# Kernel optimization log

Hardware: AMD Instinct MI355X
Metric: run time of the kernel (lower is better)

The kernel has to match this reference:

```python
import jax, jax.numpy as jnp
import numpy as np


def _lstm_cell(gates, c_prev):
    # PyTorch gate order: input, forget, cell(g), output
    i, f, g, o = jnp.split(gates, 4, axis=-1)
    c = jax.nn.sigmoid(f) * c_prev + jax.nn.sigmoid(i) * jnp.tanh(g)
    h = jax.nn.sigmoid(o) * jnp.tanh(c)
    return h, c


def setup_inputs() -> dict:
    key = jax.random.key(0)
    ks = jax.random.split(key, 20)
    s = 0.1
    x = jax.random.normal(ks[0], (1, 1, 37), dtype=jnp.float32)
    # active flags live at columns 12 + 5*opp_id; set opponents 0,2,3 active (==1)
    act_idx = 12 + 5 * jnp.arange(5)
    flags = jnp.array([1.0, 0.0, 1.0, 1.0, 0.0], dtype=jnp.float32)
    x = x.at[0, 0, act_idx].set(flags)
    inp = {
        'x': x,
        'gen_Wih': s * jax.random.normal(ks[1], (10, 40, 12), dtype=jnp.float32),
        'gen_Whh': s * jax.random.normal(ks[2], (10, 40, 10), dtype=jnp.float32),
        'gen_bih': s * jax.random.normal(ks[3], (10, 40), dtype=jnp.float32),
        'gen_bhh': s * jax.random.normal(ks[4], (10, 40), dtype=jnp.float32),
        'gen_h0': s * jax.random.normal(ks[5], (10, 10), dtype=jnp.float32),
        'gen_c0': s * jax.random.normal(ks[6], (10, 10), dtype=jnp.float32),
        'game_Wih': s * jax.random.normal(ks[7], (5, 10, 20, 4), dtype=jnp.float32),
        'game_Whh': s * jax.random.normal(ks[8], (5, 10, 20, 5), dtype=jnp.float32),
        'game_bih': s * jax.random.normal(ks[9], (5, 10, 20), dtype=jnp.float32),
        'game_bhh': s * jax.random.normal(ks[10], (5, 10, 20), dtype=jnp.float32),
        'game_h0': s * jax.random.normal(ks[11], (5, 10, 5), dtype=jnp.float32),
        'game_c0': s * jax.random.normal(ks[12], (5, 10, 5), dtype=jnp.float32),
        'W1': s * jax.random.normal(ks[13], (50, 200), dtype=jnp.float32),
        'b1': s * jax.random.normal(ks[14], (50,), dtype=jnp.float32),
        'W2': s * jax.random.normal(ks[15], (10, 50), dtype=jnp.float32),
        'b2': s * jax.random.normal(ks[16], (10,), dtype=jnp.float32),
        'W3': s * jax.random.normal(ks[17], (1, 10), dtype=jnp.float32),
        'b3': s * jax.random.normal(ks[18], (1,), dtype=jnp.float32),
    }
    return inp


def reference(x, gen_Wih, gen_Whh, gen_bih, gen_bhh, gen_h0, gen_c0,
              game_Wih, game_Whh, game_bih, game_bhh, game_h0, game_c0,
              W1, b1, W2, b2, W3, b3):
    # seq_len = batch = 1 (forced by the view(1,1,-1) -> Linear(200) shapes)
    xg = x[0, 0, :12]                                     # [12] general features
    # 10 independent LSTM(12,10) cells, batched via einsum over the cell axis k
    gates_g = (jnp.einsum('kgd,d->kg', gen_Wih, xg)
               + jnp.einsum('kgh,kh->kg', gen_Whh, gen_h0)
               + gen_bih + gen_bhh)                       # [10, 40]
    h_gen, _ = _lstm_cell(gates_g, gen_c0)                # [10, 10]
    x_gen_out = h_gen.reshape(-1)                         # [100]

    xo = x[0, 0, 12:37].reshape(5, 5)                     # 5 opponents x 5 feats
    active = xo[:, 0]                                     # active flag
    feats = xo[:, 1:]                                     # [5, 4]
    # 5 opponents x 10 independent LSTM(4,5) game cells
    gates_o = (jnp.einsum('okgd,od->okg', game_Wih, feats)
               + jnp.einsum('okgh,okh->okg', game_Whh, game_h0)
               + game_bih + game_bhh)                     # [5, 10, 20]
    h_game, _ = _lstm_cell(gates_o, game_c0)              # [5, 10, 5]
    game_flat = h_game.reshape(5, 50)
    # Bug replicated from source: the round loop concatenates x_opp_game (the
    # stale output of game-LSTM #9) 10 times; round LSTM outputs are unused.
    repeated = jnp.tile(h_game[:, 9, :], (1, 10))         # [5, 50]
    opp_single = jnp.concatenate([game_flat, repeated], axis=1)  # [5, 100]

    mask = (active == 1.0).astype(x.dtype)                # 'if x_active == 1'
    opp_avg = (mask[:, None] * opp_single).sum(0) / mask.sum()   # mean over active

    test = jnp.concatenate([x_gen_out, opp_avg])          # [200]
    h1 = jnp.tanh(test @ W1.T + b1)
    h2 = jnp.tanh(h1 @ W2.T + b2)
    out = jnp.tanh(h2 @ W3.T + b3)
    return out.reshape(1, 1, 1)
```

## Files before the change

### kernel.cpp

```cpp
#include <hip/hip_runtime.h>
#include <math.h>


__device__ __forceinline__ float fsig(float v) {
    return __fdividef(1.0f, 1.0f + __expf(-v));
}
__device__ __forceinline__ float ftanh(float v) {
    return 1.0f - __fdividef(2.0f, 1.0f + __expf(2.0f * v));
}

__global__ __launch_bounds__(1024) void net6max_kernel(
    const float* __restrict__ x,
    const float* __restrict__ gen_Wih,
    const float* __restrict__ gen_Whh,
    const float* __restrict__ gen_bih,
    const float* __restrict__ gen_bhh,
    const float* __restrict__ gen_h0,
    const float* __restrict__ gen_c0,
    const float* __restrict__ game_Wih,
    const float* __restrict__ game_Whh,
    const float* __restrict__ game_bih,
    const float* __restrict__ game_bhh,
    const float* __restrict__ game_h0,
    const float* __restrict__ game_c0,
    const float* __restrict__ W1,
    const float* __restrict__ b1,
    const float* __restrict__ W2,
    const float* __restrict__ b2,
    const float* __restrict__ W3,
    const float* __restrict__ b3,
    float* __restrict__ out)
{
    __shared__ __align__(16) float s_xg[12];
    __shared__ __align__(16) float s_feats[5][4];
    __shared__ __align__(16) float s_active[8];
    __shared__ __align__(16) float s_gates_g[400];
    __shared__ __align__(16) float s_gates_o[1000];
    __shared__ __align__(16) float s_hgame[5][10][5];
    __shared__ __align__(16) float s_test[200];
    __shared__ __align__(16) float s_h1[52];
    __shared__ __align__(16) float s_h2[12];

    const int tid = threadIdx.x;

    if (tid < 12) s_xg[tid] = x[tid];
    if (tid >= 64 && tid < 64 + 25) {
        int j = tid - 64;
        int o = j / 5, c = j % 5;
        float v = x[12 + j];
        if (c == 0) s_active[o] = v;
        else        s_feats[o][c - 1] = v;
    }
    __syncthreads();

    if (tid < 400) {
        int k = tid / 40;
        const float4* wih4 = (const float4*)(gen_Wih + (size_t)tid * 12);
        const float2* whh2 = (const float2*)(gen_Whh + (size_t)tid * 10);
        const float2* h02  = (const float2*)(gen_h0 + k * 10);
        float4 xa = *(const float4*)&s_xg[0];
        float4 xb = *(const float4*)&s_xg[4];
        float4 xc = *(const float4*)&s_xg[8];
        float4 p4 = wih4[0] * xa + wih4[1] * xb + wih4[2] * xc;
        float2 q2 = whh2[0] * h02[0] + whh2[1] * h02[1] + whh2[2] * h02[2]
                  + whh2[3] * h02[3] + whh2[4] * h02[4];
        float acc = gen_bih[tid] + gen_bhh[tid]
                  + p4.x + p4.y + p4.z + p4.w + q2.x + q2.y;
        s_gates_g[tid] = acc;
    }

    {
        int gt = -1;
        if (tid < 400)       gt = 600 + tid;
        else if (tid >= 424) gt = tid - 424;
        if (gt >= 0) {
            int o   = gt / 200;
            int ok_ = gt / 20;
            const float4* wih4 = (const float4*)(game_Wih + (size_t)gt * 4);
            const float*  whh  = game_Whh + (size_t)gt * 5;
            const float*  h0   = game_h0 + ok_ * 5;
            float4 f4 = *(const float4*)&s_feats[o][0];
            float4 p  = wih4[0] * f4;
            float acc = game_bih[gt] + game_bhh[gt] + p.x + p.y + p.z + p.w;
            acc += whh[0]*h0[0] + whh[1]*h0[1] + whh[2]*h0[2]
                 + whh[3]*h0[3] + whh[4]*h0[4];
            s_gates_o[gt] = acc;
        }
    }
    __syncthreads();

    if (tid < 100) {
        int k = tid / 10, j = tid % 10;
        int base = k * 40;
        float gi = s_gates_g[base + j];
        float gf = s_gates_g[base + 10 + j];
        float gg = s_gates_g[base + 20 + j];
        float go = s_gates_g[base + 30 + j];
        float c = fsig(gf) * gen_c0[tid] + fsig(gi) * ftanh(gg);
        s_test[tid] = fsig(go) * ftanh(c);
    } else if (tid >= 512 && tid < 512 + 250) {
        int t = tid - 512;
        int o = t / 50;
        int rem = t % 50;
        int k = rem / 5, j = rem % 5;
        int base = (o * 10 + k) * 20;
        float gi = s_gates_o[base + j];
        float gf = s_gates_o[base + 5 + j];
        float gg = s_gates_o[base + 10 + j];
        float go = s_gates_o[base + 15 + j];
        float c = fsig(gf) * game_c0[(o * 10 + k) * 5 + j] + fsig(gi) * ftanh(gg);
        s_hgame[o][k][j] = fsig(go) * ftanh(c);
    }
    __syncthreads();

    if (tid < 100) {
        float msum = 0.0f, acc = 0.0f;
        #pragma unroll
        for (int o = 0; o < 5; ++o) {
            float m = (s_active[o] == 1.0f) ? 1.0f : 0.0f;
            msum += m;
            float v = (tid < 50) ? s_hgame[o][tid / 5][tid % 5]
                                 : s_hgame[o][9][(tid - 50) % 5];
            acc += m * v;
        }
        s_test[100 + tid] = __fdividef(acc, msum);
    }
    __syncthreads();

    if (tid < 200) {
        int r = tid >> 2, q = tid & 3;
        const float4* w4 = (const float4*)(W1 + (size_t)r * 200);
        const float4* t4 = (const float4*)s_test;
        float4 acc4 = make_float4(0.f, 0.f, 0.f, 0.f);
        #pragma unroll
        for (int m = 0; m < 12; ++m) {
            int c4 = q + 4 * m;
            acc4 += w4[c4] * t4[c4];
        }
        if (q < 2) {
            int c4 = 48 + q;
            acc4 += w4[c4] * t4[c4];
        }
        float acc = acc4.x + acc4.y + acc4.z + acc4.w;
        acc += __shfl_xor(acc, 1);
        acc += __shfl_xor(acc, 2);
        if (q == 0) s_h1[r] = ftanh(acc + b1[r]);
    }
    __syncthreads();

    if (tid < 20) {
        int r = tid >> 1, q = tid & 1;
        const float2* w2 = (const float2*)(W2 + (size_t)r * 50);
        const float2* h2 = (const float2*)s_h1;
        float2 acc2 = make_float2(0.f, 0.f);
        #pragma unroll
        for (int m = 0; m < 12; ++m) {
            int c = q + 2 * m;
            acc2 += w2[c] * h2[c];
        }
        if (q == 0) acc2 += w2[24] * h2[24];
        float acc = acc2.x + acc2.y;
        acc += __shfl_xor(acc, 1);
        if (q == 0) s_h2[r] = ftanh(acc + b2[r]);
    }
    __syncthreads();

    if (tid == 0) {
        float acc = b3[0];
        #pragma unroll
        for (int c = 0; c < 10; ++c) acc += W3[c] * s_h2[c];
        out[0] = ftanh(acc);
    }
}

extern "C" void kernel_launch(void* const* d_in, const int* in_sizes, int n_in,
                              void* d_out, int out_size, void* d_ws, size_t ws_size,
                              hipStream_t stream) {
    (void)in_sizes; (void)n_in; (void)out_size; (void)d_ws; (void)ws_size;
    const float* x        = (const float*)d_in[0];
    const float* gen_Wih  = (const float*)d_in[1];
    const float* gen_Whh  = (const float*)d_in[2];
    const float* gen_bih  = (const float*)d_in[3];
    const float* gen_bhh  = (const float*)d_in[4];
    const float* gen_h0   = (const float*)d_in[5];
    const float* gen_c0   = (const float*)d_in[6];
    const float* game_Wih = (const float*)d_in[7];
    const float* game_Whh = (const float*)d_in[8];
    const float* game_bih = (const float*)d_in[9];
    const float* game_bhh = (const float*)d_in[10];
    const float* game_h0  = (const float*)d_in[11];
    const float* game_c0  = (const float*)d_in[12];
    const float* W1       = (const float*)d_in[13];
    const float* b1       = (const float*)d_in[14];
    const float* W2       = (const float*)d_in[15];
    const float* b2       = (const float*)d_in[16];
    const float* W3       = (const float*)d_in[17];
    const float* b3       = (const float*)d_in[18];
    float* out = (float*)d_out;

    net6max_kernel<<<1, 1024, 0, stream>>>(
        x, gen_Wih, gen_Whh, gen_bih, gen_bhh, gen_h0, gen_c0,
        game_Wih, game_Whh, game_bih, game_bhh, game_h0, game_c0,
        W1, b1, W2, b2, W3, b3, out);
}
```

Baseline: 10.71 us.

## Fuse LSTM gate matvecs into cell threads and shrink block to 384

Each LSTM cell thread now computes its own four gate dot products directly from global memory instead of staging gates in shared memory, which removes two barriers and the input staging step. The block shrinks from 1024 to 384 threads. The final W2 and W3 layers are merged through a warp shuffle reduction, removing one more barrier and the s_h2 buffer. Each thread now does four times the gate work serially, so the critical path gets longer per thread in exchange for fewer syncs.

```diff
diff --git a/kernel.cpp b/kernel.cpp
--- a/kernel.cpp
+++ b/kernel.cpp
@@ -9,7 +9,7 @@
     return 1.0f - __fdividef(2.0f, 1.0f + __expf(2.0f * v));
 }
 
-__global__ __launch_bounds__(1024) void net6max_kernel(
+__global__ __launch_bounds__(384) void net6max_kernel(
     const float* __restrict__ x,
     const float* __restrict__ gen_Wih,
     const float* __restrict__ gen_Whh,
@@ -31,85 +31,63 @@
     const float* __restrict__ b3,
     float* __restrict__ out)
 {
-    __shared__ __align__(16) float s_xg[12];
-    __shared__ __align__(16) float s_feats[5][4];
-    __shared__ __align__(16) float s_active[8];
-    __shared__ __align__(16) float s_gates_g[400];
-    __shared__ __align__(16) float s_gates_o[1000];
     __shared__ __align__(16) float s_hgame[5][10][5];
     __shared__ __align__(16) float s_test[200];
     __shared__ __align__(16) float s_h1[52];
-    __shared__ __align__(16) float s_h2[12];
 
     const int tid = threadIdx.x;
 
-    if (tid < 12) s_xg[tid] = x[tid];
-    if (tid >= 64 && tid < 64 + 25) {
-        int j = tid - 64;
-        int o = j / 5, c = j % 5;
-        float v = x[12 + j];
-        if (c == 0) s_active[o] = v;
-        else        s_feats[o][c - 1] = v;
-    }
-    __syncthreads();
-
-    if (tid < 400) {
-        int k = tid / 40;
-        const float4* wih4 = (const float4*)(gen_Wih + (size_t)tid * 12);
-        const float2* whh2 = (const float2*)(gen_Whh + (size_t)tid * 10);
-        const float2* h02  = (const float2*)(gen_h0 + k * 10);
-        float4 xa = *(const float4*)&s_xg[0];
-        float4 xb = *(const float4*)&s_xg[4];
-        float4 xc = *(const float4*)&s_xg[8];
-        float4 p4 = wih4[0] * xa + wih4[1] * xb + wih4[2] * xc;
-        float2 q2 = whh2[0] * h02[0] + whh2[1] * h02[1] + whh2[2] * h02[2]
-                  + whh2[3] * h02[3] + whh2[4] * h02[4];
-        float acc = gen_bih[tid] + gen_bhh[tid]
-                  + p4.x + p4.y + p4.z + p4.w + q2.x + q2.y;
-        s_gates_g[tid] = acc;
-    }
-
-    {
-        int gt = -1;
-        if (tid < 400)       gt = 600 + tid;
-        else if (tid >= 424) gt = tid - 424;
-        if (gt >= 0) {
-            int o   = gt / 200;
-            int ok_ = gt / 20;
-            const float4* wih4 = (const float4*)(game_Wih + (size_t)gt * 4);
-            const float*  whh  = game_Whh + (size_t)gt * 5;
-            const float*  h0   = game_h0 + ok_ * 5;
-            float4 f4 = *(const float4*)&s_feats[o][0];
-            float4 p  = wih4[0] * f4;
-            float acc = game_bih[gt] + game_bhh[gt] + p.x + p.y + p.z + p.w;
-            acc += whh[0]*h0[0] + whh[1]*h0[1] + whh[2]*h0[2]
-                 + whh[3]*h0[3] + whh[4]*h0[4];
-            s_gates_o[gt] = acc;
-        }
-    }
-    __syncthreads();
-
     if (tid < 100) {
         int k = tid / 10, j = tid % 10;
-        int base = k * 40;
-        float gi = s_gates_g[base + j];
-        float gf = s_gates_g[base + 10 + j];
-        float gg = s_gates_g[base + 20 + j];
-        float go = s_gates_g[base + 30 + j];
-        float c = fsig(gf) * gen_c0[tid] + fsig(gi) * ftanh(gg);
-        s_test[tid] = fsig(go) * ftanh(c);
-    } else if (tid >= 512 && tid < 512 + 250) {
-        int t = tid - 512;
-        int o = t / 50;
-        int rem = t % 50;
+        const float*  Wk  = gen_Wih + (size_t)k * 480;
+        const float*  Uk  = gen_Whh + (size_t)k * 400;
+        const float*  bi  = gen_bih + k * 40;
+        const float*  bh  = gen_bhh + k * 40;
+        const float2* h02 = (const float2*)(gen_h0 + k * 10);
+        float2 h0a = h02[0], h0b = h02[1], h0c = h02[2], h0d = h02[3], h0e = h02[4];
+        float4 xa = *(const float4*)&x[0];
+        float4 xb = *(const float4*)&x[4];
+        float4 xc = *(const float4*)&x[8];
+        float g4[4];
+        #pragma unroll
+        for (int gq = 0; gq < 4; ++gq) {
+            int r = gq * 10 + j;
+            const float4* w4 = (const float4*)(Wk + r * 12);
+            const float2* u2 = (const float2*)(Uk + r * 10);
+            float4 p = w4[0] * xa + w4[1] * xb + w4[2] * xc;
+            float2 q = u2[0] * h0a + u2[1] * h0b + u2[2] * h0c
+                     + u2[3] * h0d + u2[4] * h0e;
+            g4[gq] = bi[r] + bh[r] + p.x + p.y + p.z + p.w + q.x + q.y;
+        }
+        float c = fsig(g4[1]) * gen_c0[tid] + fsig(g4[0]) * ftanh(g4[2]);
+        s_test[tid] = fsig(g4[3]) * ftanh(c);
+    } else if (tid >= 128 && tid < 378) {
+        int u = tid - 128;
+        int o = u / 50;
+        int rem = u % 50;
         int k = rem / 5, j = rem % 5;
-        int base = (o * 10 + k) * 20;
-        float gi = s_gates_o[base + j];
-        float gf = s_gates_o[base + 5 + j];
-        float gg = s_gates_o[base + 10 + j];
-        float go = s_gates_o[base + 15 + j];
-        float c = fsig(gf) * game_c0[(o * 10 + k) * 5 + j] + fsig(gi) * ftanh(gg);
-        s_hgame[o][k][j] = fsig(go) * ftanh(c);
+        int ok = o * 10 + k;
+        const float* Wk = game_Wih + (size_t)ok * 80;
+        const float* Uk = game_Whh + (size_t)ok * 100;
+        const float* bi = game_bih + ok * 20;
+        const float* bh = game_bhh + ok * 20;
+        const float* h0 = game_h0 + ok * 5;
+        float h00 = h0[0], h01 = h0[1], h02_ = h0[2], h03 = h0[3], h04 = h0[4];
+        const float* fx = x + 13 + 5 * o;
+        float f0 = fx[0], f1 = fx[1], f2 = fx[2], f3 = fx[3];
+        float g4[4];
+        #pragma unroll
+        for (int gq = 0; gq < 4; ++gq) {
+            int r = gq * 5 + j;
+            float4 w = *(const float4*)(Wk + r * 4);
+            const float* uu = Uk + r * 5;
+            float acc = bi[r] + bh[r]
+                      + w.x * f0 + w.y * f1 + w.z * f2 + w.w * f3;
+            acc += uu[0]*h00 + uu[1]*h01 + uu[2]*h02_ + uu[3]*h03 + uu[4]*h04;
+            g4[gq] = acc;
+        }
+        float c = fsig(g4[1]) * game_c0[ok * 5 + j] + fsig(g4[0]) * ftanh(g4[2]);
+        s_hgame[o][k][j] = fsig(g4[3]) * ftanh(c);
     }
     __syncthreads();
 
@@ -117,10 +95,10 @@
         float msum = 0.0f, acc = 0.0f;
         #pragma unroll
         for (int o = 0; o < 5; ++o) {
-            float m = (s_active[o] == 1.0f) ? 1.0f : 0.0f;
+            float m = (x[12 + 5 * o] == 1.0f) ? 1.0f : 0.0f;
             msum += m;
             float v = (tid < 50) ? s_hgame[o][tid / 5][tid % 5]
-                                 : s_hgame[o][9][(tid - 50) % 5];
+                                 : s_hgame[o][9][tid % 5];
             acc += m * v;
         }
         s_test[100 + tid] = __fdividef(acc, msum);
@@ -148,28 +126,29 @@
     }
     __syncthreads();
 
-    if (tid < 20) {
-        int r = tid >> 1, q = tid & 1;
-        const float2* w2 = (const float2*)(W2 + (size_t)r * 50);
-        const float2* h2 = (const float2*)s_h1;
-        float2 acc2 = make_float2(0.f, 0.f);
-        #pragma unroll
-        for (int m = 0; m < 12; ++m) {
-            int c = q + 2 * m;
-            acc2 += w2[c] * h2[c];
+    if (tid < 32) {
+        float acc = 0.f;
+        if (tid < 20) {
+            int r = tid >> 1, q = tid & 1;
+            const float2* w2 = (const float2*)(W2 + (size_t)r * 50);
+            const float2* h1v = (const float2*)s_h1;
+            float2 acc2 = make_float2(0.f, 0.f);
+            #pragma unroll
+            for (int m = 0; m < 12; ++m) {
+                int c = q + 2 * m;
+                acc2 += w2[c] * h1v[c];
+            }
+            if (q == 0) acc2 += w2[24] * h1v[24];
+            float a = acc2.x + acc2.y;
+            a += __shfl_xor(a, 1);
+            acc = (q == 0) ? ftanh(a + b2[r]) * W3[r] : 0.f;
         }
-        if (q == 0) acc2 += w2[24] * h2[24];
-        float acc = acc2.x + acc2.y;
+        acc += __shfl_xor(acc, 2);
+        acc += __shfl_xor(acc, 4);
+        acc += __shfl_xor(acc, 8);
+        acc += __shfl_xor(acc, 16);
         acc += __shfl_xor(acc, 1);
-        if (q == 0) s_h2[r] = ftanh(acc + b2[r]);
-    }
-    __syncthreads();
-
-    if (tid == 0) {
-        float acc = b3[0];
-        #pragma unroll
-        for (int c = 0; c < 10; ++c) acc += W3[c] * s_h2[c];
-        out[0] = ftanh(acc);
+        if (tid == 0) out[0] = ftanh(acc + b3[0]);
     }
 }
 
@@ -198,7 +177,7 @@
     const float* b3       = (const float*)d_in[18];
     float* out = (float*)d_out;
 
-    net6max_kernel<<<1, 1024, 0, stream>>>(
+    net6max_kernel<<<1, 384, 0, stream>>>(
         x, gen_Wih, gen_Whh, gen_bih, gen_bhh, gen_h0, gen_c0,
         game_Wih, game_Whh, game_bih, game_bhh, game_h0, game_c0,
         W1, b1, W2, b2, W3, b3, out);
```

Result: faster. 9.558 us (-10.7%).

## Prefetch MLP weights into LDS early and drop staging syncs

Applied to the files above, without the earlier changes.

Loads W1 and W2 into shared memory during the gate-computation phase, so their global-memory latency overlaps with the LSTM work instead of sitting on the later serial MLP path. Removes the initial shared staging of x and its barrier by reading x straight from global memory. Fuses the final W3 dot product into the W2 stage with a warp shuffle reduction, removing one barrier and a serial loop. The cost is a larger LDS footprint and more global loads issued at the start, plus a padded W1 row stride to avoid bank conflicts.

```diff
diff --git a/kernel.cpp b/kernel.cpp
--- a/kernel.cpp
+++ b/kernel.cpp
@@ -31,44 +31,30 @@
     const float* __restrict__ b3,
     float* __restrict__ out)
 {
-    __shared__ __align__(16) float s_xg[12];
-    __shared__ __align__(16) float s_feats[5][4];
-    __shared__ __align__(16) float s_active[8];
+    __shared__ __align__(16) float4 s_W1v[50 * 51];
+    __shared__ __align__(16) float2 s_W2v[10 * 25];
     __shared__ __align__(16) float s_gates_g[400];
     __shared__ __align__(16) float s_gates_o[1000];
     __shared__ __align__(16) float s_hgame[5][10][5];
     __shared__ __align__(16) float s_test[200];
     __shared__ __align__(16) float s_h1[52];
-    __shared__ __align__(16) float s_h2[12];
 
     const int tid = threadIdx.x;
-
-    if (tid < 12) s_xg[tid] = x[tid];
-    if (tid >= 64 && tid < 64 + 25) {
-        int j = tid - 64;
-        int o = j / 5, c = j % 5;
-        float v = x[12 + j];
-        if (c == 0) s_active[o] = v;
-        else        s_feats[o][c - 1] = v;
-    }
-    __syncthreads();
 
     if (tid < 400) {
         int k = tid / 40;
         const float4* wih4 = (const float4*)(gen_Wih + (size_t)tid * 12);
         const float2* whh2 = (const float2*)(gen_Whh + (size_t)tid * 10);
         const float2* h02  = (const float2*)(gen_h0 + k * 10);
-        float4 xa = *(const float4*)&s_xg[0];
-        float4 xb = *(const float4*)&s_xg[4];
-        float4 xc = *(const float4*)&s_xg[8];
+        float4 xa = *(const float4*)&x[0];
+        float4 xb = *(const float4*)&x[4];
+        float4 xc = *(const float4*)&x[8];
         float4 p4 = wih4[0] * xa + wih4[1] * xb + wih4[2] * xc;
         float2 q2 = whh2[0] * h02[0] + whh2[1] * h02[1] + whh2[2] * h02[2]
                   + whh2[3] * h02[3] + whh2[4] * h02[4];
-        float acc = gen_bih[tid] + gen_bhh[tid]
-                  + p4.x + p4.y + p4.z + p4.w + q2.x + q2.y;
-        s_gates_g[tid] = acc;
-    }
-
+        s_gates_g[tid] = gen_bih[tid] + gen_bhh[tid]
+                       + p4.x + p4.y + p4.z + p4.w + q2.x + q2.y;
+    }
     {
         int gt = -1;
         if (tid < 400)       gt = 600 + tid;
@@ -79,12 +65,32 @@
             const float4* wih4 = (const float4*)(game_Wih + (size_t)gt * 4);
             const float*  whh  = game_Whh + (size_t)gt * 5;
             const float*  h0   = game_h0 + ok_ * 5;
-            float4 f4 = *(const float4*)&s_feats[o][0];
-            float4 p  = wih4[0] * f4;
-            float acc = game_bih[gt] + game_bhh[gt] + p.x + p.y + p.z + p.w;
+            const float*  fx   = x + 13 + 5 * o;
+            float4 w = wih4[0];
+            float acc = game_bih[gt] + game_bhh[gt]
+                      + w.x * fx[0] + w.y * fx[1] + w.z * fx[2] + w.w * fx[3];
             acc += whh[0]*h0[0] + whh[1]*h0[1] + whh[2]*h0[2]
                  + whh[3]*h0[3] + whh[4]*h0[4];
             s_gates_o[gt] = acc;
+        }
+    }
+    {
+        const float4* W1v = (const float4*)W1;
+        #pragma unroll
+        for (int t = 0; t < 3; ++t) {
+            int i = tid + t * 1024;
+            if (i < 2500) {
+                int row = i / 50, c4 = i % 50;
+                s_W1v[row * 51 + c4] = W1v[i];
+            }
+        }
+    }
+    if (tid >= 400 && tid < 424) {
+        const float2* W2v = (const float2*)W2;
+        #pragma unroll
+        for (int t = 0; t < 11; ++t) {
+            int i = (tid - 400) + 24 * t;
+            if (i < 250) s_W2v[i] = W2v[i];
         }
     }
     __syncthreads();
@@ -98,7 +104,7 @@
         float go = s_gates_g[base + 30 + j];
         float c = fsig(gf) * gen_c0[tid] + fsig(gi) * ftanh(gg);
         s_test[tid] = fsig(go) * ftanh(c);
-    } else if (tid >= 512 && tid < 512 + 250) {
+    } else if (tid >= 512 && tid < 762) {
         int t = tid - 512;
         int o = t / 50;
         int rem = t % 50;
@@ -117,10 +123,10 @@
         float msum = 0.0f, acc = 0.0f;
         #pragma unroll
         for (int o = 0; o < 5; ++o) {
-            float m = (s_active[o] == 1.0f) ? 1.0f : 0.0f;
+            float m = (x[12 + 5 * o] == 1.0f) ? 1.0f : 0.0f;
             msum += m;
             float v = (tid < 50) ? s_hgame[o][tid / 5][tid % 5]
-                                 : s_hgame[o][9][(tid - 50) % 5];
+                                 : s_hgame[o][9][tid % 5];
             acc += m * v;
         }
         s_test[100 + tid] = __fdividef(acc, msum);
@@ -129,7 +135,7 @@
 
     if (tid < 200) {
         int r = tid >> 2, q = tid & 3;
-        const float4* w4 = (const float4*)(W1 + (size_t)r * 200);
+        const float4* w4 = &s_W1v[r * 51];
         const float4* t4 = (const float4*)s_test;
         float4 acc4 = make_float4(0.f, 0.f, 0.f, 0.f);
         #pragma unroll
@@ -148,28 +154,29 @@
     }
     __syncthreads();
 
-    if (tid < 20) {
-        int r = tid >> 1, q = tid & 1;
-        const float2* w2 = (const float2*)(W2 + (size_t)r * 50);
-        const float2* h2 = (const float2*)s_h1;
-        float2 acc2 = make_float2(0.f, 0.f);
-        #pragma unroll
-        for (int m = 0; m < 12; ++m) {
-            int c = q + 2 * m;
-            acc2 += w2[c] * h2[c];
-        }
-        if (q == 0) acc2 += w2[24] * h2[24];
-        float acc = acc2.x + acc2.y;
+    if (tid < 32) {
+        float acc = 0.f;
+        if (tid < 20) {
+            int r = tid >> 1, q = tid & 1;
+            const float2* w2 = &s_W2v[r * 25];
+            const float2* h1v = (const float2*)s_h1;
+            float2 acc2 = make_float2(0.f, 0.f);
+            #pragma unroll
+            for (int m = 0; m < 12; ++m) {
+                int c = q + 2 * m;
+                acc2 += w2[c] * h1v[c];
+            }
+            if (q == 0) acc2 += w2[24] * h1v[24];
+            float a = acc2.x + acc2.y;
+            a += __shfl_xor(a, 1);
+            acc = (q == 0) ? ftanh(a + b2[r]) * W3[r] : 0.f;
+        }
+        acc += __shfl_xor(acc, 2);
+        acc += __shfl_xor(acc, 4);
+        acc += __shfl_xor(acc, 8);
+        acc += __shfl_xor(acc, 16);
         acc += __shfl_xor(acc, 1);
-        if (q == 0) s_h2[r] = ftanh(acc + b2[r]);
-    }
-    __syncthreads();
-
-    if (tid == 0) {
-        float acc = b3[0];
-        #pragma unroll
-        for (int c = 0; c < 10; ++c) acc += W3[c] * s_h2[c];
-        out[0] = ftanh(acc);
+        if (tid == 0) out[0] = ftanh(acc + b3[0]);
     }
 }
 
```

After: 9.986 us. 1.07x faster.
